# Optimization experiments

Hardware: AMD Instinct MI355X
Metric: run time of the kernel (lower is better)

The kernel has to match this reference:

```python
import jax, jax.numpy as jnp
import numpy as np

N = 100000
E = 1600000
IN_DIM, HID, Z = 128, 64, 32


def gcn_conv(x, src, dst, num_nodes, W, b):
    """PyG GCNConv: add self-loops, symmetric deg^-1/2 normalization.
    x: [N, F_in]; src/dst: [E] int (self-loops already appended by caller wrapper).
    """
    h = x @ W  # [N, F_out] transform first (PyG order)
    ones = jnp.ones(src.shape[0], dtype=x.dtype)
    deg = jax.ops.segment_sum(ones, dst, num_segments=num_nodes)  # in-degree incl. self-loop
    dinv = jnp.where(deg > 0, jax.lax.rsqrt(deg), 0.0)
    norm = dinv[src] * dinv[dst]  # [E]
    msgs = h[src] * norm[:, None]  # [E, F_out] irregular gather
    out = jax.ops.segment_sum(msgs, dst, num_segments=num_nodes)  # scatter-add
    return out + b


def setup_inputs() -> dict:
    key = jax.random.key(0)
    ks = jax.random.split(key, 10)
    x = jax.random.normal(ks[0], (N, IN_DIM), dtype=jnp.float32)
    edge_index = jax.random.randint(ks[1], (2, E), 0, N, dtype=jnp.int64)

    def glorot(k, fan_in, fan_out):
        s = jnp.sqrt(6.0 / (fan_in + fan_out))
        return jax.random.uniform(k, (fan_in, fan_out), jnp.float32, -s, s)

    return {
        "x": x,
        "edge_index": edge_index,
        "W1": glorot(ks[2], IN_DIM, HID),
        "b1": jnp.zeros((HID,), jnp.float32),
        "W2": glorot(ks[3], HID, Z),
        "b2": jnp.zeros((Z,), jnp.float32),
        "Wmu": glorot(ks[4], Z, Z),
        "bmu": jnp.zeros((Z,), jnp.float32),
        "Wlv": glorot(ks[5], Z, Z),
        "blv": jnp.zeros((Z,), jnp.float32),
    }


def reference(x, edge_index, W1, b1, W2, b2, Wmu, bmu, Wlv, blv):
    num_nodes = x.shape[0]
    loop = jnp.arange(num_nodes, dtype=edge_index.dtype)
    src = jnp.concatenate([edge_index[0], loop])  # self-loops appended
    dst = jnp.concatenate([edge_index[1], loop])
    h = jax.nn.relu(gcn_conv(x, src, dst, num_nodes, W1, b1))
    h = gcn_conv(h, src, dst, num_nodes, W2, b2)
    mu = h @ Wmu + bmu
    logvar = h @ Wlv + blv
    return (mu, logvar)
```

## Files before the change

kernel.cpp:

```cpp
#include <hip/hip_runtime.h>

#define N_NODES 100000
#define N_EDGES 1600000
#define IN_F   128
#define HID_F  64
#define Z_F    32
#define NBUK   782
#define BCAP   3072
#define P1T    4096
#define P1_BLOCKS ((N_EDGES + P1T - 1) / P1T)
#define AGG_CAP 2048

typedef unsigned int uint32;
typedef __attribute__((ext_vector_type(8))) short bf16x8;
typedef __attribute__((ext_vector_type(4))) float f32x4;

__device__ __forceinline__ unsigned short f2bf(float f) {
    unsigned u = __float_as_uint(f);
    u = (u + 0x7FFF + ((u >> 16) & 1)) >> 16;
    return (unsigned short)u;
}
__device__ __forceinline__ float bflo(uint32 u) { return __uint_as_float(u << 16); }
__device__ __forceinline__ float bfhi(uint32 u) { return __uint_as_float(u & 0xFFFF0000u); }

__global__ __launch_bounds__(256) void phase1_kernel(const int* __restrict__ ei,
                                                     int* __restrict__ gcur,
                                                     uint32* __restrict__ pairs) {
    __shared__ int hist[NBUK];
    __shared__ int lbase[NBUK];
    __shared__ int gbase[NBUK];
    __shared__ int lcur[NBUK];
    __shared__ uint32 stage[P1T];
    __shared__ unsigned short sbid[P1T];
    __shared__ int part[256];
    int tid = threadIdx.x;
    int e0 = blockIdx.x * P1T;
    int ecnt = N_EDGES - e0; if (ecnt > P1T) ecnt = P1T;
    for (int b = tid; b < NBUK; b += 256) { hist[b] = 0; lcur[b] = 0; }
    __syncthreads();
    for (int k = tid; k < ecnt; k += 256)
        atomicAdd(&hist[ei[N_EDGES + e0 + k] >> 7], 1);
    __syncthreads();
    int t4 = tid * 4;
    int l0 = 0, l1 = 0, l2 = 0, l3 = 0, s = 0;
    if (t4 + 0 < NBUK) { l0 = hist[t4 + 0]; s += l0; }
    if (t4 + 1 < NBUK) { l1 = hist[t4 + 1]; s += l1; }
    if (t4 + 2 < NBUK) { l2 = hist[t4 + 2]; s += l2; }
    if (t4 + 3 < NBUK) { l3 = hist[t4 + 3]; s += l3; }
    part[tid] = s;
    __syncthreads();
    for (int off = 1; off < 256; off <<= 1) {
        int add = (tid >= off) ? part[tid - off] : 0;
        __syncthreads();
        part[tid] += add;
        __syncthreads();
    }
    int run = part[tid] - s;
    if (t4 + 0 < NBUK) { lbase[t4 + 0] = run; run += l0; }
    if (t4 + 1 < NBUK) { lbase[t4 + 1] = run; run += l1; }
    if (t4 + 2 < NBUK) { lbase[t4 + 2] = run; run += l2; }
    if (t4 + 3 < NBUK) { lbase[t4 + 3] = run; run += l3; }
    for (int b = tid; b < NBUK; b += 256) {
        int h = hist[b];
        gbase[b] = h ? atomicAdd(&gcur[b], h) : 0;
    }
    __syncthreads();
    for (int k = tid; k < ecnt; k += 256) {
        int sN = ei[e0 + k];
        int d  = ei[N_EDGES + e0 + k];
        int b = d >> 7;
        int slot = lbase[b] + atomicAdd(&lcur[b], 1);
        stage[slot] = (uint32)sN | ((uint32)(d & 127) << 17);
        sbid[slot] = (unsigned short)b;
    }
    __syncthreads();
    for (int k = tid; k < ecnt; k += 256) {
        int b = sbid[k];
        int r = gbase[b] + (k - lbase[b]);
        if (r < BCAP) pairs[(size_t)b * BCAP + r] = stage[k];
    }
}

__global__ void prep_kernel(const int* __restrict__ gcur,
                            const float* __restrict__ W1, const float* __restrict__ W2,
                            const float* __restrict__ Wmu, const float* __restrict__ Wlv,
                            int* __restrict__ bucketBase, int* __restrict__ rowptr,
                            unsigned short* __restrict__ Wt1,
                            unsigned short* __restrict__ Wt2,
                            unsigned short* __restrict__ Wth) {
    __shared__ int s[1024];
    int t = threadIdx.x;
    int v = (t < NBUK) ? gcur[t] : 0;
    s[t] = v;
    __syncthreads();
    for (int off = 1; off < 1024; off <<= 1) {
        int add = (t >= off) ? s[t - off] : 0;
        __syncthreads();
        s[t] += add;
        __syncthreads();
    }
    if (t < NBUK) bucketBase[t] = s[t] - v;
    if (t == 0) rowptr[N_NODES] = N_EDGES;
    for (int i = t; i < IN_F * HID_F; i += 1024) {
        int n = i >> 7, k = i & 127;
        Wt1[i] = f2bf(W1[k * HID_F + n]);
    }
    for (int i = t; i < HID_F * Z_F; i += 1024) {
        int n = i >> 6, k = i & 63;
        Wt2[i] = f2bf(W2[k * Z_F + n]);
    }
    for (int i = t; i < Z_F * 64; i += 1024) {
        int n = i >> 5, k = i & 31;
        Wth[i] = f2bf(n < 32 ? Wmu[k * Z_F + n] : Wlv[k * Z_F + (n - 32)]);
    }
}

__global__ __launch_bounds__(256) void phase2_kernel(const uint32* __restrict__ pairs,
                                                     const int* __restrict__ gcur,
                                                     const int* __restrict__ bucketBase,
                                                     int* __restrict__ rowptr,
                                                     float* __restrict__ dinv,
                                                     int* __restrict__ col) {
    __shared__ int lhist[128];
    __shared__ int lscan[128];
    __shared__ int lcur[128];
    __shared__ int stage[BCAP];
    int b = blockIdx.x;
    int tid = threadIdx.x;
    int cnt_b = gcur[b];
    if (cnt_b > BCAP) cnt_b = BCAP;
    int gbase = bucketBase[b];
    int node0 = b << 7;
    int nb = N_NODES - node0;
    if (nb > 128) nb = 128;
    if (tid < 128) { lhist[tid] = 0; lcur[tid] = 0; }
    __syncthreads();
    const uint32* pb = pairs + (size_t)b * BCAP;
    for (int k = tid; k < cnt_b; k += 256) atomicAdd(&lhist[pb[k] >> 17], 1);
    __syncthreads();
    int v = (tid < 128) ? lhist[tid] : 0;
    if (tid < 128) lscan[tid] = v;
    __syncthreads();
    for (int off = 1; off < 128; off <<= 1) {
        int add = (tid < 128 && tid >= off) ? lscan[tid - off] : 0;
        __syncthreads();
        if (tid < 128) lscan[tid] += add;
        __syncthreads();
    }
    if (tid < 128) lscan[tid] -= v;
    __syncthreads();
    if (tid < nb) {
        rowptr[node0 + tid] = gbase + lscan[tid];
        dinv[node0 + tid] = rsqrtf((float)(lhist[tid] + 1));
    }
    for (int k = tid; k < cnt_b; k += 256) {
        uint32 u = pb[k];
        int ld = u >> 17;
        int r = atomicAdd(&lcur[ld], 1);
        stage[lscan[ld] + r] = (int)(u & 0x1FFFF);
    }
    __syncthreads();
    for (int k = tid; k < cnt_b; k += 256) col[gbase + k] = stage[k];
}

__global__ __launch_bounds__(256) void gemm1_kernel(const float* __restrict__ x,
                                                    const unsigned short* __restrict__ Wt1,
                                                    const float* __restrict__ dinv,
                                                    unsigned short* __restrict__ t1) {
    __shared__ unsigned short Cs[64 * 72];
    __shared__ float dv[64];
    int tid = threadIdx.x;
    int node0 = blockIdx.x * 64;
    if (tid < 64) {
        int n = node0 + tid;
        dv[tid] = (n < N_NODES) ? dinv[n] : 0.f;
    }
    __syncthreads();
    int w = tid >> 6, lane = tid & 63;
    int m = lane & 15, quad = lane >> 4;
    int row = w * 16 + m;
    int node = node0 + row;
    const float* xr = x + (size_t)min(node, N_NODES - 1) * IN_F;
    f32x4 acc0 = {0.f, 0.f, 0.f, 0.f};
    f32x4 acc1 = acc0, acc2 = acc0, acc3 = acc0;
#pragma unroll
    for (int ks = 0; ks < 4; ks++) {
        int kb = ks * 32 + quad * 8;
        float4 f0 = *(const float4*)(xr + kb);
        float4 f1 = *(const float4*)(xr + kb + 4);
        union { bf16x8 v; unsigned short u[8]; } A;
        A.u[0] = f2bf(f0.x); A.u[1] = f2bf(f0.y); A.u[2] = f2bf(f0.z); A.u[3] = f2bf(f0.w);
        A.u[4] = f2bf(f1.x); A.u[5] = f2bf(f1.y); A.u[6] = f2bf(f1.z); A.u[7] = f2bf(f1.w);
        bf16x8 b0 = *(const bf16x8*)&Wt1[(0 * 16 + m) * IN_F + kb];
        bf16x8 b1 = *(const bf16x8*)&Wt1[(1 * 16 + m) * IN_F + kb];
        bf16x8 b2 = *(const bf16x8*)&Wt1[(2 * 16 + m) * IN_F + kb];
        bf16x8 b3 = *(const bf16x8*)&Wt1[(3 * 16 + m) * IN_F + kb];
        acc0 = __builtin_amdgcn_mfma_f32_16x16x32_bf16(A.v, b0, acc0, 0, 0, 0);
        acc1 = __builtin_amdgcn_mfma_f32_16x16x32_bf16(A.v, b1, acc1, 0, 0, 0);
        acc2 = __builtin_amdgcn_mfma_f32_16x16x32_bf16(A.v, b2, acc2, 0, 0, 0);
        acc3 = __builtin_amdgcn_mfma_f32_16x16x32_bf16(A.v, b3, acc3, 0, 0, 0);
    }
    int rbase = w * 16 + quad * 4;
#pragma unroll
    for (int reg = 0; reg < 4; reg++) {
        int r = rbase + reg;
        float d = dv[r];
        Cs[r * 72 +  0 + m] = f2bf(acc0[reg] * d);
        Cs[r * 72 + 16 + m] = f2bf(acc1[reg] * d);
        Cs[r * 72 + 32 + m] = f2bf(acc2[reg] * d);
        Cs[r * 72 + 48 + m] = f2bf(acc3[reg] * d);
    }
    __syncthreads();
#pragma unroll
    for (int it = 0; it < 4; it++) {
        int idx = it * 256 + tid;
        int r = idx >> 4, c = idx & 15;
        int nd = node0 + r;
        if (nd < N_NODES) {
            uint2 vv = *(const uint2*)&Cs[r * 72 + c * 4];
            *(uint2*)&t1[(size_t)nd * HID_F + c * 4] = vv;
        }
    }
}

__global__ __launch_bounds__(256) void agg1_kernel(const unsigned short* __restrict__ t1,
                                                   const int* __restrict__ rowptr,
                                                   const int* __restrict__ col,
                                                   const float* __restrict__ dinv,
                                                   const float* __restrict__ b1,
                                                   float* __restrict__ h1) {
    __shared__ int lcol[AGG_CAP];
    __shared__ int lrp[65];
    __shared__ float ldv[64];
    int tid = threadIdx.x;
    int node0 = blockIdx.x * 64;
    if (tid < 65) lrp[tid] = rowptr[min(node0 + tid, N_NODES)];
    __syncthreads();
    int s0 = lrp[0];
    int cnt = lrp[64] - s0; if (cnt > AGG_CAP) cnt = AGG_CAP;
    for (int k = tid; k < cnt; k += 256) lcol[k] = col[s0 + k];
    if (tid < 64) {
        int n = node0 + tid;
        ldv[tid] = (n < N_NODES) ? dinv[n] : 0.f;
    }
    __syncthreads();
    int lane = tid & 63, w = tid >> 6;
    int q = lane >> 4, fl = lane & 15;
    int qg = w * 4 + q;
    const uint2* t1v = (const uint2*)t1;
    float4 bb = ((const float4*)b1)[fl];
#pragma unroll
    for (int rep = 0; rep < 4; rep++) {
        int li = qg + rep * 16;
        int node = node0 + li;
        if (node >= N_NODES) break;
        int s = lrp[li] - s0;
        int e = lrp[li + 1] - s0; if (e > cnt) e = cnt;
        float a0 = 0.f, a1 = 0.f, a2 = 0.f, a3 = 0.f;
        int p = s;
        for (; p + 3 < e; p += 4) {
            int c0 = lcol[p], c1 = lcol[p + 1], c2 = lcol[p + 2], c3 = lcol[p + 3];
            uint2 u0 = t1v[(size_t)c0 * 16 + fl];
            uint2 u1 = t1v[(size_t)c1 * 16 + fl];
            uint2 u2 = t1v[(size_t)c2 * 16 + fl];
            uint2 u3 = t1v[(size_t)c3 * 16 + fl];
            a0 += bflo(u0.x) + bflo(u1.x) + bflo(u2.x) + bflo(u3.x);
            a1 += bfhi(u0.x) + bfhi(u1.x) + bfhi(u2.x) + bfhi(u3.x);
            a2 += bflo(u0.y) + bflo(u1.y) + bflo(u2.y) + bflo(u3.y);
            a3 += bfhi(u0.y) + bfhi(u1.y) + bfhi(u2.y) + bfhi(u3.y);
        }
        for (; p < e; p++) {
            uint2 u = t1v[(size_t)lcol[p] * 16 + fl];
            a0 += bflo(u.x); a1 += bfhi(u.x);
            a2 += bflo(u.y); a3 += bfhi(u.y);
        }
        uint2 us = t1v[(size_t)node * 16 + fl];
        float di = ldv[li];
        float4 o;
        o.x = fmaxf(di * (a0 + bflo(us.x)) + bb.x, 0.f);
        o.y = fmaxf(di * (a1 + bfhi(us.x)) + bb.y, 0.f);
        o.z = fmaxf(di * (a2 + bflo(us.y)) + bb.z, 0.f);
        o.w = fmaxf(di * (a3 + bfhi(us.y)) + bb.w, 0.f);
        ((float4*)(h1 + (size_t)node * HID_F))[fl] = o;
    }
}

__global__ __launch_bounds__(256) void gemm2_kernel(const float* __restrict__ h1,
                                                    const unsigned short* __restrict__ Wt2,
                                                    const float* __restrict__ dinv,
                                                    unsigned short* __restrict__ t2s) {
    __shared__ unsigned short Cs[64 * 36];
    __shared__ float dv[64];
    int tid = threadIdx.x;
    int node0 = blockIdx.x * 64;
    if (tid < 64) {
        int n = node0 + tid;
        dv[tid] = (n < N_NODES) ? dinv[n] : 0.f;
    }
    __syncthreads();
    int w = tid >> 6, lane = tid & 63;
    int m = lane & 15, quad = lane >> 4;
    int node = node0 + w * 16 + m;
    const float* hr = h1 + (size_t)min(node, N_NODES - 1) * HID_F;
    f32x4 acc0 = {0.f, 0.f, 0.f, 0.f};
    f32x4 acc1 = acc0;
#pragma unroll
    for (int ks = 0; ks < 2; ks++) {
        int kb = ks * 32 + quad * 8;
        float4 f0 = *(const float4*)(hr + kb);
        float4 f1 = *(const float4*)(hr + kb + 4);
        union { bf16x8 v; unsigned short u[8]; } A;
        A.u[0] = f2bf(f0.x); A.u[1] = f2bf(f0.y); A.u[2] = f2bf(f0.z); A.u[3] = f2bf(f0.w);
        A.u[4] = f2bf(f1.x); A.u[5] = f2bf(f1.y); A.u[6] = f2bf(f1.z); A.u[7] = f2bf(f1.w);
        bf16x8 b0 = *(const bf16x8*)&Wt2[(0 * 16 + m) * HID_F + kb];
        bf16x8 b1 = *(const bf16x8*)&Wt2[(1 * 16 + m) * HID_F + kb];
        acc0 = __builtin_amdgcn_mfma_f32_16x16x32_bf16(A.v, b0, acc0, 0, 0, 0);
        acc1 = __builtin_amdgcn_mfma_f32_16x16x32_bf16(A.v, b1, acc1, 0, 0, 0);
    }
    int rbase = w * 16 + quad * 4;
#pragma unroll
    for (int reg = 0; reg < 4; reg++) {
        int r = rbase + reg;
        float d = dv[r];
        Cs[r * 36 +  0 + m] = f2bf(acc0[reg] * d);
        Cs[r * 36 + 16 + m] = f2bf(acc1[reg] * d);
    }
    __syncthreads();
#pragma unroll
    for (int it = 0; it < 2; it++) {
        int idx = it * 256 + tid;
        int r = idx >> 3, c = idx & 7;
        int nd = node0 + r;
        if (nd < N_NODES) {
            uint2 vv = *(const uint2*)&Cs[r * 36 + c * 4];
            *(uint2*)&t2s[(size_t)nd * Z_F + c * 4] = vv;
        }
    }
}

__global__ __launch_bounds__(256) void agg2_kernel(const unsigned short* __restrict__ t2s,
                                                   const int* __restrict__ rowptr,
                                                   const int* __restrict__ col,
                                                   const float* __restrict__ dinv,
                                                   const float* __restrict__ b2,
                                                   float* __restrict__ h2) {
    __shared__ int lcol[AGG_CAP];
    __shared__ int lrp[65];
    __shared__ float ldv[64];
    int tid = threadIdx.x;
    int node0 = blockIdx.x * 64;
    if (tid < 65) lrp[tid] = rowptr[min(node0 + tid, N_NODES)];
    __syncthreads();
    int s0 = lrp[0];
    int cnt = lrp[64] - s0; if (cnt > AGG_CAP) cnt = AGG_CAP;
    for (int k = tid; k < cnt; k += 256) lcol[k] = col[s0 + k];
    if (tid < 64) {
        int n = node0 + tid;
        ldv[tid] = (n < N_NODES) ? dinv[n] : 0.f;
    }
    __syncthreads();
    int lane = tid & 63, w = tid >> 6;
    int oc = lane >> 3, fo = lane & 7;
    int og = w * 8 + oc;
    const uint2* t2v = (const uint2*)t2s;
    float4 bb = ((const float4*)b2)[fo];
#pragma unroll
    for (int rep = 0; rep < 2; rep++) {
        int li = og + rep * 32;
        int node = node0 + li;
        if (node >= N_NODES) break;
        int s = lrp[li] - s0;
        int e = lrp[li + 1] - s0; if (e > cnt) e = cnt;
        float a0 = 0.f, a1 = 0.f, a2 = 0.f, a3 = 0.f;
        int p = s;
        for (; p + 3 < e; p += 4) {
            int c0 = lcol[p], c1 = lcol[p + 1], c2 = lcol[p + 2], c3 = lcol[p + 3];
            uint2 u0 = t2v[(size_t)c0 * 8 + fo];
            uint2 u1 = t2v[(size_t)c1 * 8 + fo];
            uint2 u2 = t2v[(size_t)c2 * 8 + fo];
            uint2 u3 = t2v[(size_t)c3 * 8 + fo];
            a0 += bflo(u0.x) + bflo(u1.x) + bflo(u2.x) + bflo(u3.x);
            a1 += bfhi(u0.x) + bfhi(u1.x) + bfhi(u2.x) + bfhi(u3.x);
            a2 += bflo(u0.y) + bflo(u1.y) + bflo(u2.y) + bflo(u3.y);
            a3 += bfhi(u0.y) + bfhi(u1.y) + bfhi(u2.y) + bfhi(u3.y);
        }
        for (; p < e; p++) {
            uint2 u = t2v[(size_t)lcol[p] * 8 + fo];
            a0 += bflo(u.x); a1 += bfhi(u.x);
            a2 += bflo(u.y); a3 += bfhi(u.y);
        }
        uint2 us = t2v[(size_t)node * 8 + fo];
        float di = ldv[li];
        float4 o;
        o.x = di * (a0 + bflo(us.x)) + bb.x;
        o.y = di * (a1 + bfhi(us.x)) + bb.y;
        o.z = di * (a2 + bflo(us.y)) + bb.z;
        o.w = di * (a3 + bfhi(us.y)) + bb.w;
        ((float4*)(h2 + (size_t)node * Z_F))[fo] = o;
    }
}

__global__ __launch_bounds__(256) void heads_kernel(const float* __restrict__ h2,
                                                    const unsigned short* __restrict__ Wth,
                                                    const float* __restrict__ bmu,
                                                    const float* __restrict__ blv,
                                                    float* __restrict__ out) {
    __shared__ float Cf[64 * 68];
    __shared__ float bias[64];
    int tid = threadIdx.x;
    int node0 = blockIdx.x * 64;
    if (tid < 32) bias[tid] = bmu[tid];
    else if (tid < 64) bias[tid] = blv[tid - 32];
    __syncthreads();
    int w = tid >> 6, lane = tid & 63;
    int m = lane & 15, quad = lane >> 4;
    int node = node0 + w * 16 + m;
    const float* hr = h2 + (size_t)min(node, N_NODES - 1) * Z_F;
    int kb = quad * 8;
    float4 f0 = *(const float4*)(hr + kb);
    float4 f1 = *(const float4*)(hr + kb + 4);
    union { bf16x8 v; unsigned short u[8]; } A;
    A.u[0] = f2bf(f0.x); A.u[1] = f2bf(f0.y); A.u[2] = f2bf(f0.z); A.u[3] = f2bf(f0.w);
    A.u[4] = f2bf(f1.x); A.u[5] = f2bf(f1.y); A.u[6] = f2bf(f1.z); A.u[7] = f2bf(f1.w);
    f32x4 acc0 = {0.f, 0.f, 0.f, 0.f};
    f32x4 acc1 = acc0, acc2 = acc0, acc3 = acc0;
    bf16x8 b0 = *(const bf16x8*)&Wth[(0 * 16 + m) * Z_F + kb];
    bf16x8 b1 = *(const bf16x8*)&Wth[(1 * 16 + m) * Z_F + kb];
    bf16x8 b2 = *(const bf16x8*)&Wth[(2 * 16 + m) * Z_F + kb];
    bf16x8 b3 = *(const bf16x8*)&Wth[(3 * 16 + m) * Z_F + kb];
    acc0 = __builtin_amdgcn_mfma_f32_16x16x32_bf16(A.v, b0, acc0, 0, 0, 0);
    acc1 = __builtin_amdgcn_mfma_f32_16x16x32_bf16(A.v, b1, acc1, 0, 0, 0);
    acc2 = __builtin_amdgcn_mfma_f32_16x16x32_bf16(A.v, b2, acc2, 0, 0, 0);
    acc3 = __builtin_amdgcn_mfma_f32_16x16x32_bf16(A.v, b3, acc3, 0, 0, 0);
    int rbase = w * 16 + quad * 4;
#pragma unroll
    for (int reg = 0; reg < 4; reg++) {
        int r = rbase + reg;
        Cf[r * 68 +  0 + m] = acc0[reg] + bias[ 0 + m];
        Cf[r * 68 + 16 + m] = acc1[reg] + bias[16 + m];
        Cf[r * 68 + 32 + m] = acc2[reg] + bias[32 + m];
        Cf[r * 68 + 48 + m] = acc3[reg] + bias[48 + m];
    }
    __syncthreads();
#pragma unroll
    for (int it = 0; it < 2; it++) {
        int idx = it * 256 + tid;
        int r = idx >> 3, c = idx & 7;
        int nd = node0 + r;
        if (nd < N_NODES) {
            float4 vmu = *(const float4*)&Cf[r * 68 + c * 4];
            float4 vlv = *(const float4*)&Cf[r * 68 + 32 + c * 4];
            *(float4*)&out[(size_t)nd * Z_F + c * 4] = vmu;
            *(float4*)&out[(size_t)N_NODES * Z_F + (size_t)nd * Z_F + c * 4] = vlv;
        }
    }
}

extern "C" void kernel_launch(void* const* d_in, const int* in_sizes, int n_in,
                              void* d_out, int out_size, void* d_ws, size_t ws_size,
                              hipStream_t stream) {
    const float* x   = (const float*)d_in[0];
    const int*   ei  = (const int*)d_in[1];
    const float* W1  = (const float*)d_in[2];
    const float* b1  = (const float*)d_in[3];
    const float* W2  = (const float*)d_in[4];
    const float* b2  = (const float*)d_in[5];
    const float* Wmu = (const float*)d_in[6];
    const float* bmu = (const float*)d_in[7];
    const float* Wlv = (const float*)d_in[8];
    const float* blv = (const float*)d_in[9];
    float* out = (float*)d_out;

    char* ws = (char*)d_ws;
    size_t off = 0;
    auto A = [&](size_t bytes) {
        size_t r = off;
        off += (bytes + 255) & ~(size_t)255;
        return r;
    };
    int*   gcur       = (int*)(ws + A((size_t)NBUK * 4));
    int*   bucketBase = (int*)(ws + A((size_t)NBUK * 4));
    int*   rowptr     = (int*)(ws + A((size_t)(N_NODES + 1) * 4));
    float* dinv       = (float*)(ws + A((size_t)N_NODES * 4));
    unsigned short* Wt1 = (unsigned short*)(ws + A((size_t)IN_F * HID_F * 2));
    unsigned short* Wt2 = (unsigned short*)(ws + A((size_t)HID_F * Z_F * 2));
    unsigned short* Wth = (unsigned short*)(ws + A((size_t)Z_F * 64 * 2));
    int*   col        = (int*)(ws + A((size_t)N_EDGES * 4));
    char*  reg1 = ws + A((size_t)NBUK * BCAP * 4);
    uint32* pairs = (uint32*)reg1;
    unsigned short* t2s = (unsigned short*)reg1;
    char*  reg2 = ws + A((size_t)N_NODES * HID_F * 2);
    unsigned short* t1 = (unsigned short*)reg2;
    float* h2 = (float*)reg2;
    float* h1 = (float*)(ws + A((size_t)N_NODES * HID_F * 4));

    hipMemsetAsync(gcur, 0, (size_t)NBUK * 4, stream);

    phase1_kernel<<<P1_BLOCKS, 256, 0, stream>>>(ei, gcur, pairs);
    prep_kernel<<<1, 1024, 0, stream>>>(gcur, W1, W2, Wmu, Wlv, bucketBase, rowptr,
                                        Wt1, Wt2, Wth);
    phase2_kernel<<<NBUK, 256, 0, stream>>>(pairs, gcur, bucketBase, rowptr, dinv, col);

    int nblk = (N_NODES + 63) / 64;
    gemm1_kernel<<<nblk, 256, 0, stream>>>(x, Wt1, dinv, t1);
    agg1_kernel<<<nblk, 256, 0, stream>>>(t1, rowptr, col, dinv, b1, h1);
    gemm2_kernel<<<nblk, 256, 0, stream>>>(h1, Wt2, dinv, t2s);
    agg2_kernel<<<nblk, 256, 0, stream>>>(t2s, rowptr, col, dinv, b2, h2);
    heads_kernel<<<nblk, 256, 0, stream>>>(h2, Wth, bmu, blv, out);
}
```

Measured before the change: 240.5 us.

## Fuse aggregation with following dense transforms via shared-memory bf16 tiles

Merges the layer-1 aggregation with the second GEMM, and the layer-2 aggregation with the mu/logvar heads. Each aggregated 64-node tile is kept in LDS as bf16 and fed straight to MFMA, so the fp32 h1/h2 round-trips through global memory and two kernel launches disappear. In exchange each block uses more LDS, which may lower occupancy in the latency-bound gather phase. The intermediates are also rounded to bf16 once when written to LDS, which matches the conversion the old GEMM kernels did on load.

```diff
diff --git a/kernel.cpp b/kernel.cpp
--- a/kernel.cpp
+++ b/kernel.cpp
@@ -19,6 +19,9 @@
     unsigned u = __float_as_uint(f);
     u = (u + 0x7FFF + ((u >> 16) & 1)) >> 16;
     return (unsigned short)u;
+}
+__device__ __forceinline__ uint32 pack2bf(float lo, float hi) {
+    return (uint32)f2bf(lo) | ((uint32)f2bf(hi) << 16);
 }
 __device__ __forceinline__ float bflo(uint32 u) { return __uint_as_float(u << 16); }
 __device__ __forceinline__ float bfhi(uint32 u) { return __uint_as_float(u & 0xFFFF0000u); }
@@ -223,15 +226,18 @@
     }
 }
 
-__global__ __launch_bounds__(256) void agg1_kernel(const unsigned short* __restrict__ t1,
-                                                   const int* __restrict__ rowptr,
-                                                   const int* __restrict__ col,
-                                                   const float* __restrict__ dinv,
-                                                   const float* __restrict__ b1,
-                                                   float* __restrict__ h1) {
+__global__ __launch_bounds__(256) void agg1gemm2_kernel(const unsigned short* __restrict__ t1,
+                                                        const int* __restrict__ rowptr,
+                                                        const int* __restrict__ col,
+                                                        const float* __restrict__ dinv,
+                                                        const float* __restrict__ b1,
+                                                        const unsigned short* __restrict__ Wt2,
+                                                        unsigned short* __restrict__ t2s) {
     __shared__ int lcol[AGG_CAP];
     __shared__ int lrp[65];
     __shared__ float ldv[64];
+    __shared__ unsigned short h1s[64 * 72];
+    __shared__ unsigned short Cs[64 * 36];
     int tid = threadIdx.x;
     int node0 = blockIdx.x * 64;
     if (tid < 65) lrp[tid] = rowptr[min(node0 + tid, N_NODES)];
@@ -253,75 +259,58 @@
     for (int rep = 0; rep < 4; rep++) {
         int li = qg + rep * 16;
         int node = node0 + li;
-        if (node >= N_NODES) break;
-        int s = lrp[li] - s0;
-        int e = lrp[li + 1] - s0; if (e > cnt) e = cnt;
-        float a0 = 0.f, a1 = 0.f, a2 = 0.f, a3 = 0.f;
-        int p = s;
-        for (; p + 3 < e; p += 4) {
-            int c0 = lcol[p], c1 = lcol[p + 1], c2 = lcol[p + 2], c3 = lcol[p + 3];
-            uint2 u0 = t1v[(size_t)c0 * 16 + fl];
-            uint2 u1 = t1v[(size_t)c1 * 16 + fl];
-            uint2 u2 = t1v[(size_t)c2 * 16 + fl];
-            uint2 u3 = t1v[(size_t)c3 * 16 + fl];
-            a0 += bflo(u0.x) + bflo(u1.x) + bflo(u2.x) + bflo(u3.x);
-            a1 += bfhi(u0.x) + bfhi(u1.x) + bfhi(u2.x) + bfhi(u3.x);
-            a2 += bflo(u0.y) + bflo(u1.y) + bflo(u2.y) + bflo(u3.y);
-            a3 += bfhi(u0.y) + bfhi(u1.y) + bfhi(u2.y) + bfhi(u3.y);
+        uint2 pk = make_uint2(0u, 0u);
+        if (node < N_NODES) {
+            int s = lrp[li] - s0;
+            int e = lrp[li + 1] - s0; if (e > cnt) e = cnt;
+            float a0 = 0.f, a1 = 0.f, a2 = 0.f, a3 = 0.f;
+            int p = s;
+            for (; p + 3 < e; p += 4) {
+                int c0 = lcol[p], c1 = lcol[p + 1], c2 = lcol[p + 2], c3 = lcol[p + 3];
+                uint2 u0 = t1v[(size_t)c0 * 16 + fl];
+                uint2 u1 = t1v[(size_t)c1 * 16 + fl];
+                uint2 u2 = t1v[(size_t)c2 * 16 + fl];
+                uint2 u3 = t1v[(size_t)c3 * 16 + fl];
+                a0 += bflo(u0.x) + bflo(u1.x) + bflo(u2.x) + bflo(u3.x);
+                a1 += bfhi(u0.x) + bfhi(u1.x) + bfhi(u2.x) + bfhi(u3.x);
+                a2 += bflo(u0.y) + bflo(u1.y) + bflo(u2.y) + bflo(u3.y);
+                a3 += bfhi(u0.y) + bfhi(u1.y) + bfhi(u2.y) + bfhi(u3.y);
+            }
+            for (; p < e; p++) {
+                uint2 u = t1v[(size_t)lcol[p] * 16 + fl];
+                a0 += bflo(u.x); a1 += bfhi(u.x);
+                a2 += bflo(u.y); a3 += bfhi(u.y);
+            }
+            uint2 us = t1v[(size_t)node * 16 + fl];
+            float di = ldv[li];
+            float o0 = fmaxf(di * (a0 + bflo(us.x)) + bb.x, 0.f);
+            float o1 = fmaxf(di * (a1 + bfhi(us.x)) + bb.y, 0.f);
+            float o2 = fmaxf(di * (a2 + bflo(us.y)) + bb.z, 0.f);
+            float o3 = fmaxf(di * (a3 + bfhi(us.y)) + bb.w, 0.f);
+            pk.x = pack2bf(o0, o1);
+            pk.y = pack2bf(o2, o3);
         }
-        for (; p < e; p++) {
-            uint2 u = t1v[(size_t)lcol[p] * 16 + fl];
-            a0 += bflo(u.x); a1 += bfhi(u.x);
-            a2 += bflo(u.y); a3 += bfhi(u.y);
-        }
-        uint2 us = t1v[(size_t)node * 16 + fl];
-        float di = ldv[li];
-        float4 o;
-        o.x = fmaxf(di * (a0 + bflo(us.x)) + bb.x, 0.f);
-        o.y = fmaxf(di * (a1 + bfhi(us.x)) + bb.y, 0.f);
-        o.z = fmaxf(di * (a2 + bflo(us.y)) + bb.z, 0.f);
-        o.w = fmaxf(di * (a3 + bfhi(us.y)) + bb.w, 0.f);
-        ((float4*)(h1 + (size_t)node * HID_F))[fl] = o;
-    }
-}
-
-__global__ __launch_bounds__(256) void gemm2_kernel(const float* __restrict__ h1,
-                                                    const unsigned short* __restrict__ Wt2,
-                                                    const float* __restrict__ dinv,
-                                                    unsigned short* __restrict__ t2s) {
-    __shared__ unsigned short Cs[64 * 36];
-    __shared__ float dv[64];
-    int tid = threadIdx.x;
-    int node0 = blockIdx.x * 64;
-    if (tid < 64) {
-        int n = node0 + tid;
-        dv[tid] = (n < N_NODES) ? dinv[n] : 0.f;
-    }
-    __syncthreads();
-    int w = tid >> 6, lane = tid & 63;
+        *(uint2*)&h1s[li * 72 + fl * 4] = pk;
+    }
+    __syncthreads();
     int m = lane & 15, quad = lane >> 4;
-    int node = node0 + w * 16 + m;
-    const float* hr = h1 + (size_t)min(node, N_NODES - 1) * HID_F;
+    int row = w * 16 + m;
     f32x4 acc0 = {0.f, 0.f, 0.f, 0.f};
     f32x4 acc1 = acc0;
 #pragma unroll
     for (int ks = 0; ks < 2; ks++) {
         int kb = ks * 32 + quad * 8;
-        float4 f0 = *(const float4*)(hr + kb);
-        float4 f1 = *(const float4*)(hr + kb + 4);
-        union { bf16x8 v; unsigned short u[8]; } A;
-        A.u[0] = f2bf(f0.x); A.u[1] = f2bf(f0.y); A.u[2] = f2bf(f0.z); A.u[3] = f2bf(f0.w);
-        A.u[4] = f2bf(f1.x); A.u[5] = f2bf(f1.y); A.u[6] = f2bf(f1.z); A.u[7] = f2bf(f1.w);
+        bf16x8 a  = *(const bf16x8*)&h1s[row * 72 + kb];
         bf16x8 b0 = *(const bf16x8*)&Wt2[(0 * 16 + m) * HID_F + kb];
         bf16x8 b1 = *(const bf16x8*)&Wt2[(1 * 16 + m) * HID_F + kb];
-        acc0 = __builtin_amdgcn_mfma_f32_16x16x32_bf16(A.v, b0, acc0, 0, 0, 0);
-        acc1 = __builtin_amdgcn_mfma_f32_16x16x32_bf16(A.v, b1, acc1, 0, 0, 0);
+        acc0 = __builtin_amdgcn_mfma_f32_16x16x32_bf16(a, b0, acc0, 0, 0, 0);
+        acc1 = __builtin_amdgcn_mfma_f32_16x16x32_bf16(a, b1, acc1, 0, 0, 0);
     }
     int rbase = w * 16 + quad * 4;
 #pragma unroll
     for (int reg = 0; reg < 4; reg++) {
         int r = rbase + reg;
-        float d = dv[r];
+        float d = ldv[r];
         Cs[r * 36 +  0 + m] = f2bf(acc0[reg] * d);
         Cs[r * 36 + 16 + m] = f2bf(acc1[reg] * d);
     }
@@ -338,18 +327,26 @@
     }
 }
 
-__global__ __launch_bounds__(256) void agg2_kernel(const unsigned short* __restrict__ t2s,
-                                                   const int* __restrict__ rowptr,
-                                                   const int* __restrict__ col,
-                                                   const float* __restrict__ dinv,
-                                                   const float* __restrict__ b2,
-                                                   float* __restrict__ h2) {
+__global__ __launch_bounds__(256) void agg2heads_kernel(const unsigned short* __restrict__ t2s,
+                                                        const int* __restrict__ rowptr,
+                                                        const int* __restrict__ col,
+                                                        const float* __restrict__ dinv,
+                                                        const float* __restrict__ b2,
+                                                        const unsigned short* __restrict__ Wth,
+                                                        const float* __restrict__ bmu,
+                                                        const float* __restrict__ blv,
+                                                        float* __restrict__ out) {
     __shared__ int lcol[AGG_CAP];
     __shared__ int lrp[65];
     __shared__ float ldv[64];
+    __shared__ unsigned short h2s[64 * 40];
+    __shared__ float Cf[64 * 68];
+    __shared__ float bias[64];
     int tid = threadIdx.x;
     int node0 = blockIdx.x * 64;
     if (tid < 65) lrp[tid] = rowptr[min(node0 + tid, N_NODES)];
+    else if (tid >= 96 && tid < 128) bias[tid - 96] = bmu[tid - 96];
+    else if (tid >= 128 && tid < 160) bias[tid - 96] = blv[tid - 128];
     __syncthreads();
     int s0 = lrp[0];
     int cnt = lrp[64] - s0; if (cnt > AGG_CAP) cnt = AGG_CAP;
@@ -368,70 +365,54 @@
     for (int rep = 0; rep < 2; rep++) {
         int li = og + rep * 32;
         int node = node0 + li;
-        if (node >= N_NODES) break;
-        int s = lrp[li] - s0;
-        int e = lrp[li + 1] - s0; if (e > cnt) e = cnt;
-        float a0 = 0.f, a1 = 0.f, a2 = 0.f, a3 = 0.f;
-        int p = s;
-        for (; p + 3 < e; p += 4) {
-            int c0 = lcol[p], c1 = lcol[p + 1], c2 = lcol[p + 2], c3 = lcol[p + 3];
-            uint2 u0 = t2v[(size_t)c0 * 8 + fo];
-            uint2 u1 = t2v[(size_t)c1 * 8 + fo];
-            uint2 u2 = t2v[(size_t)c2 * 8 + fo];
-            uint2 u3 = t2v[(size_t)c3 * 8 + fo];
-            a0 += bflo(u0.x) + bflo(u1.x) + bflo(u2.x) + bflo(u3.x);
-            a1 += bfhi(u0.x) + bfhi(u1.x) + bfhi(u2.x) + bfhi(u3.x);
-            a2 += bflo(u0.y) + bflo(u1.y) + bflo(u2.y) + bflo(u3.y);
-            a3 += bfhi(u0.y) + bfhi(u1.y) + bfhi(u2.y) + bfhi(u3.y);
+        uint2 pk = make_uint2(0u, 0u);
+        if (node < N_NODES) {
+            int s = lrp[li] - s0;
+            int e = lrp[li + 1] - s0; if (e > cnt) e = cnt;
+            float a0 = 0.f, a1 = 0.f, a2 = 0.f, a3 = 0.f;
+            int p = s;
+            for (; p + 3 < e; p += 4) {
+                int c0 = lcol[p], c1 = lcol[p + 1], c2 = lcol[p + 2], c3 = lcol[p + 3];
+                uint2 u0 = t2v[(size_t)c0 * 8 + fo];
+                uint2 u1 = t2v[(size_t)c1 * 8 + fo];
+                uint2 u2 = t2v[(size_t)c2 * 8 + fo];
+                uint2 u3 = t2v[(size_t)c3 * 8 + fo];
+                a0 += bflo(u0.x) + bflo(u1.x) + bflo(u2.x) + bflo(u3.x);
+                a1 += bfhi(u0.x) + bfhi(u1.x) + bfhi(u2.x) + bfhi(u3.x);
+                a2 += bflo(u0.y) + bflo(u1.y) + bflo(u2.y) + bflo(u3.y);
+                a3 += bfhi(u0.y) + bfhi(u1.y) + bfhi(u2.y) + bfhi(u3.y);
+            }
+            for (; p < e; p++) {
+                uint2 u = t2v[(size_t)lcol[p] * 8 + fo];
+                a0 += bflo(u.x); a1 += bfhi(u.x);
+                a2 += bflo(u.y); a3 += bfhi(u.y);
+            }
+            uint2 us = t2v[(size_t)node * 8 + fo];
+            float di = ldv[li];
+            float o0 = di * (a0 + bflo(us.x)) + bb.x;
+            float o1 = di * (a1 + bfhi(us.x)) + bb.y;
+            float o2 = di * (a2 + bflo(us.y)) + bb.z;
+            float o3 = di * (a3 + bfhi(us.y)) + bb.w;
+            pk.x = pack2bf(o0, o1);
+            pk.y = pack2bf(o2, o3);
         }
-        for (; p < e; p++) {
-            uint2 u = t2v[(size_t)lcol[p] * 8 + fo];
-            a0 += bflo(u.x); a1 += bfhi(u.x);
-            a2 += bflo(u.y); a3 += bfhi(u.y);
-        }
-        uint2 us = t2v[(size_t)node * 8 + fo];
-        float di = ldv[li];
-        float4 o;
-        o.x = di * (a0 + bflo(us.x)) + bb.x;
-        o.y = di * (a1 + bfhi(us.x)) + bb.y;
-        o.z = di * (a2 + bflo(us.y)) + bb.z;
-        o.w = di * (a3 + bfhi(us.y)) + bb.w;
-        ((float4*)(h2 + (size_t)node * Z_F))[fo] = o;
-    }
-}
-
-__global__ __launch_bounds__(256) void heads_kernel(const float* __restrict__ h2,
-                                                    const unsigned short* __restrict__ Wth,
-                                                    const float* __restrict__ bmu,
-                                                    const float* __restrict__ blv,
-                                                    float* __restrict__ out) {
-    __shared__ float Cf[64 * 68];
-    __shared__ float bias[64];
-    int tid = threadIdx.x;
-    int node0 = blockIdx.x * 64;
-    if (tid < 32) bias[tid] = bmu[tid];
-    else if (tid < 64) bias[tid] = blv[tid - 32];
-    __syncthreads();
-    int w = tid >> 6, lane = tid & 63;
+        *(uint2*)&h2s[li * 40 + fo * 4] = pk;
+    }
+    __syncthreads();
     int m = lane & 15, quad = lane >> 4;
-    int node = node0 + w * 16 + m;
-    const float* hr = h2 + (size_t)min(node, N_NODES - 1) * Z_F;
+    int row = w * 16 + m;
     int kb = quad * 8;
-    float4 f0 = *(const float4*)(hr + kb);
-    float4 f1 = *(const float4*)(hr + kb + 4);
-    union { bf16x8 v; unsigned short u[8]; } A;
-    A.u[0] = f2bf(f0.x); A.u[1] = f2bf(f0.y); A.u[2] = f2bf(f0.z); A.u[3] = f2bf(f0.w);
-    A.u[4] = f2bf(f1.x); A.u[5] = f2bf(f1.y); A.u[6] = f2bf(f1.z); A.u[7] = f2bf(f1.w);
+    bf16x8 a  = *(const bf16x8*)&h2s[row * 40 + kb];
+    bf16x8 b0 = *(const bf16x8*)&Wth[(0 * 16 + m) * Z_F + kb];
+    bf16x8 b1 = *(const bf16x8*)&Wth[(1 * 16 + m) * Z_F + kb];
+    bf16x8 b2v = *(const bf16x8*)&Wth[(2 * 16 + m) * Z_F + kb];
+    bf16x8 b3 = *(const bf16x8*)&Wth[(3 * 16 + m) * Z_F + kb];
     f32x4 acc0 = {0.f, 0.f, 0.f, 0.f};
     f32x4 acc1 = acc0, acc2 = acc0, acc3 = acc0;
-    bf16x8 b0 = *(const bf16x8*)&Wth[(0 * 16 + m) * Z_F + kb];
-    bf16x8 b1 = *(const bf16x8*)&Wth[(1 * 16 + m) * Z_F + kb];
-    bf16x8 b2 = *(const bf16x8*)&Wth[(2 * 16 + m) * Z_F + kb];
-    bf16x8 b3 = *(const bf16x8*)&Wth[(3 * 16 + m) * Z_F + kb];
-    acc0 = __builtin_amdgcn_mfma_f32_16x16x32_bf16(A.v, b0, acc0, 0, 0, 0);
-    acc1 = __builtin_amdgcn_mfma_f32_16x16x32_bf16(A.v, b1, acc1, 0, 0, 0);
-    acc2 = __builtin_amdgcn_mfma_f32_16x16x32_bf16(A.v, b2, acc2, 0, 0, 0);
-    acc3 = __builtin_amdgcn_mfma_f32_16x16x32_bf16(A.v, b3, acc3, 0, 0, 0);
+    acc0 = __builtin_amdgcn_mfma_f32_16x16x32_bf16(a, b0, acc0, 0, 0, 0);
+    acc1 = __builtin_amdgcn_mfma_f32_16x16x32_bf16(a, b1, acc1, 0, 0, 0);
+    acc2 = __builtin_amdgcn_mfma_f32_16x16x32_bf16(a, b2v, acc2, 0, 0, 0);
+    acc3 = __builtin_amdgcn_mfma_f32_16x16x32_bf16(a, b3, acc3, 0, 0, 0);
     int rbase = w * 16 + quad * 4;
 #pragma unroll
     for (int reg = 0; reg < 4; reg++) {
@@ -489,10 +470,7 @@
     char*  reg1 = ws + A((size_t)NBUK * BCAP * 4);
     uint32* pairs = (uint32*)reg1;
     unsigned short* t2s = (unsigned short*)reg1;
-    char*  reg2 = ws + A((size_t)N_NODES * HID_F * 2);
-    unsigned short* t1 = (unsigned short*)reg2;
-    float* h2 = (float*)reg2;
-    float* h1 = (float*)(ws + A((size_t)N_NODES * HID_F * 4));
+    unsigned short* t1 = (unsigned short*)(ws + A((size_t)N_NODES * HID_F * 2));
 
     hipMemsetAsync(gcur, 0, (size_t)NBUK * 4, stream);
 
@@ -503,8 +481,6 @@
 
     int nblk = (N_NODES + 63) / 64;
     gemm1_kernel<<<nblk, 256, 0, stream>>>(x, Wt1, dinv, t1);
-    agg1_kernel<<<nblk, 256, 0, stream>>>(t1, rowptr, col, dinv, b1, h1);
-    gemm2_kernel<<<nblk, 256, 0, stream>>>(h1, Wt2, dinv, t2s);
-    agg2_kernel<<<nblk, 256, 0, stream>>>(t2s, rowptr, col, dinv, b2, h2);
-    heads_kernel<<<nblk, 256, 0, stream>>>(h2, Wth, bmu, blv, out);
-}
+    agg1gemm2_kernel<<<nblk, 256, 0, stream>>>(t1, rowptr, col, dinv, b1, Wt2, t2s);
+    agg2heads_kernel<<<nblk, 256, 0, stream>>>(t2s, rowptr, col, dinv, b2, Wth, bmu, blv, out);
+}
```

Measured after the change: 228.2 us. 5.1% less time.
